# Performance work log

Measured on AMD Instinct MI355X. Metric: run time of the kernel, lower is better.

## Reference

```python
import jax, jax.numpy as jnp
import numpy as np

ALPHA = 0.2  # LeakyReLU slope
S1, S2 = 5, 10  # neighbor sample sizes, hard-coded in the torch forward

N, F, D, C, B = 100000, 512, 256, 40, 16384


def setup_inputs() -> dict:
    key = jax.random.key(0)
    ks = jax.random.split(key, 7)
    x = jax.random.normal(ks[0], (N, F), dtype=jnp.float32)
    # xavier-like scaling for the weights
    W1 = jax.random.normal(ks[1], (D, F), dtype=jnp.float32) * (2.0 / (D + F)) ** 0.5
    W2 = jax.random.normal(ks[2], (D, D), dtype=jnp.float32) * (2.0 / (D + D)) ** 0.5
    Wc = jax.random.normal(ks[3], (C, D), dtype=jnp.float32) * (2.0 / (C + D)) ** 0.5
    nodes = jax.random.randint(ks[4], (B,), 0, N, dtype=jnp.int32)
    neigh1 = jax.random.randint(ks[5], (N, S1), 0, N, dtype=jnp.int32)
    neigh2 = jax.random.randint(ks[6], (B, S2), 0, N, dtype=jnp.int32)
    return {"x": x, "W1": W1, "W2": W2, "Wc": Wc,
            "nodes": nodes, "neigh1": neigh1, "neigh2": neigh2}


def leaky_relu(v):
    return jnp.where(v >= 0, v, ALPHA * v)


def reference(x, W1, W2, Wc, nodes, neigh1, neigh2):
    # Layer 1 (MeanAggregator, gcn=True): mean over sampled neighbors + self,
    # then linear transform + LeakyReLU. Computed for all N nodes.
    agg1 = (x[neigh1].sum(axis=1) + x) / (S1 + 1)          # [N, F]
    h1 = leaky_relu(agg1 @ W1.T)                            # [N, D]
    # Layer 2: mean over sampled neighbors + self, on batch nodes.
    agg2 = (h1[neigh2].sum(axis=1) + h1[nodes]) / (S2 + 1)  # [B, D]
    h2 = leaky_relu(agg2 @ W2.T)                            # [B, D]
    # scores = self.weight.mm(x_2.t()).t()
    scores = h2 @ Wc.T                                      # [B, C]
    return scores
```

## Files before the change

### kernel.cpp

```cpp
#include <hip/hip_runtime.h>
#include <hip/hip_bf16.h>


#define NN 100000
#define FF 512
#define DD 256
#define BB 16384
#define CC 40

typedef __attribute__((ext_vector_type(8))) short bf16x8;
typedef __attribute__((ext_vector_type(4))) float f32x4;
typedef unsigned short u16;
typedef unsigned int u32;
typedef __attribute__((ext_vector_type(4))) u32 u32x4;

__device__ __forceinline__ float bf_lo(u32 u) { u32 v = u << 16; float f; __builtin_memcpy(&f, &v, 4); return f; }
__device__ __forceinline__ float bf_hi(u32 u) { u32 v = u & 0xffff0000u; float f; __builtin_memcpy(&f, &v, 4); return f; }
__device__ __forceinline__ float2 bf2f(u32 u) { return make_float2(bf_lo(u), bf_hi(u)); }
__device__ __forceinline__ float asf(u32 u) { float f; __builtin_memcpy(&f, &u, 4); return f; }
__device__ __forceinline__ u32 packbf2(float a, float b) {
  __hip_bfloat162 h = __float22bfloat162_rn(make_float2(a, b));
  u32 u; __builtin_memcpy(&u, &h, 4); return u;
}
__device__ __forceinline__ u16 fbits(float v) {
  __hip_bfloat16 h = __float2bfloat16(v);
  u16 u; __builtin_memcpy(&u, &h, 2); return u;
}
__device__ __forceinline__ float lrelu(float v) { return v >= 0.f ? v : 0.2f * v; }
__device__ __forceinline__ int swz(int r, int c) { return r * 128 + ((c ^ (r & 7)) << 4); }
__device__ __forceinline__ void gld_lds16(const u16* g, void* l) {
  __builtin_amdgcn_global_load_lds((const __attribute__((address_space(1))) unsigned int*)g,
                                   (__attribute__((address_space(3))) unsigned int*)l, 16, 0, 0);
}
__device__ __forceinline__ u32x4 ld4(const float* p) { return *(const u32x4*)p; }

__global__ __launch_bounds__(256) void k0_cvt(
    const float* __restrict__ W1, const float* __restrict__ W2, const float* __restrict__ Wc,
    u16* __restrict__ w1b, u16* __restrict__ w2b, u16* __restrict__ wcb,
    u32* __restrict__ flagw)
{
  const int i = blockIdx.x * 256 + threadIdx.x;
  if (i < 25024) flagw[i] = 0;
  const float* src; u16* dst; int r, cc, rowE;
  if (i < 16384)      { src = W1; dst = w1b; r = i >> 6; cc = i & 63; rowE = 512; }
  else if (i < 24576) { int j = i - 16384; src = W2; dst = w2b; r = j >> 5; cc = j & 31; rowE = 256; }
  else if (i < 25856) { int j = i - 24576; src = Wc; dst = wcb; r = j >> 5; cc = j & 31; rowE = 256; }
  else return;
  const int g = cc >> 3, cp = cc & 7;
  const float* s = src + (u32)r * rowE + g * 64 + (u32)(cp ^ (r & 7)) * 8;
  const float4 v0 = *(const float4*)s;
  const float4 v1 = *(const float4*)(s + 4);
  uint4 o;
  o.x = packbf2(v0.x, v0.y); o.y = packbf2(v0.z, v0.w);
  o.z = packbf2(v1.x, v1.y); o.w = packbf2(v1.z, v1.w);
  *(uint4*)(dst + (u32)r * rowE + g * 64 + cp * 8) = o;
}

__global__ __launch_bounds__(256) void k0b_flags(
    const int* __restrict__ nodes, const int* __restrict__ neigh2,
    unsigned char* __restrict__ flags)
{
  const int i = blockIdx.x * 256 + threadIdx.x;
  int idx;
  if (i < BB) idx = nodes[i];
  else if (i < BB + BB * 10) idx = neigh2[i - BB];
  else return;
  flags[idx] = 1;
}

__global__ __launch_bounds__(512, 4) void k1_gemm(
    const float* __restrict__ x, const u16* __restrict__ w1b, u16* __restrict__ z)
{
  __shared__ __align__(16) unsigned char lds[65536];

  const int t = threadIdx.x;
  const int rowBase = blockIdx.x * 128;
  const int lane = t & 63, w = t >> 6;
  const int lr = lane & 15, kg = lane >> 4;

  int rw = rowBase + w * 16 + lr; if (rw > NN - 1) rw = NN - 1;
  const float* xr = x + (u32)rw * FF + (u32)kg * 8;

  const u32 bofs = (u32)(w * 8 + (lane >> 3)) * FF + (u32)(lane & 7) * 8;

  int bvb[2];
#pragma unroll
  for (int kk = 0; kk < 2; ++kk)
    bvb[kk] = lr * 128 + (((kk * 4 + kg) ^ (lr & 7)) << 4);

  f32x4 acc[16];
#pragma unroll
  for (int n = 0; n < 16; ++n) acc[n] = (f32x4)0.0f;

  u32x4 pa[2][2];
#pragma unroll
  for (int kk = 0; kk < 2; ++kk) {
    pa[kk][0] = ld4(xr + kk * 32);
    pa[kk][1] = ld4(xr + kk * 32 + 4);
  }
#pragma unroll
  for (int i = 0; i < 4; ++i)
    gld_lds16(w1b + bofs + (u32)i * 64 * FF, lds + w * 1024 + i * 8192);
#pragma unroll
  for (int i = 0; i < 4; ++i)
    gld_lds16(w1b + bofs + (u32)i * 64 * FF + 64, lds + 32768 + w * 1024 + i * 8192);

#pragma unroll
  for (int ks = 0; ks < 8; ++ks) {
    bf16x8 av[2];
#pragma unroll
    for (int kk = 0; kk < 2; ++kk) {
      u32x4 p;
      p[0] = packbf2(asf(pa[kk][0][0]), asf(pa[kk][0][1]));
      p[1] = packbf2(asf(pa[kk][0][2]), asf(pa[kk][0][3]));
      p[2] = packbf2(asf(pa[kk][1][0]), asf(pa[kk][1][1]));
      p[3] = packbf2(asf(pa[kk][1][2]), asf(pa[kk][1][3]));
      av[kk] = *(bf16x8*)&p;
    }
    if (ks < 7) {
#pragma unroll
      for (int kk = 0; kk < 2; ++kk) {
        pa[kk][0] = ld4(xr + (u32)(ks + 1) * 64 + kk * 32);
        pa[kk][1] = ld4(xr + (u32)(ks + 1) * 64 + kk * 32 + 4);
      }
      asm volatile("s_waitcnt vmcnt(8)" ::: "memory");
    } else {
      asm volatile("s_waitcnt vmcnt(0)" ::: "memory");
    }
    __builtin_amdgcn_sched_barrier(0);
    __builtin_amdgcn_s_barrier();
    __builtin_amdgcn_sched_barrier(0);

    const int bo = (ks & 1) * 32768;
#pragma unroll
    for (int kk = 0; kk < 2; ++kk)
#pragma unroll
      for (int n = 0; n < 16; ++n) {
        const bf16x8 bv = *(const bf16x8*)(lds + bo + bvb[kk] + n * 2048);
        acc[n] = __builtin_amdgcn_mfma_f32_16x16x32_bf16(bv, av[kk], acc[n], 0, 0, 0);
      }
    __builtin_amdgcn_sched_barrier(0);
    __builtin_amdgcn_s_barrier();
    __builtin_amdgcn_sched_barrier(0);
    if (ks <= 5) {
      unsigned char* bl = lds + bo + w * 1024;
#pragma unroll
      for (int i = 0; i < 4; ++i)
        gld_lds16(w1b + bofs + (u32)i * 64 * FF + (u32)(ks + 2) * 64, bl + i * 8192);
    }
  }

  __syncthreads();
  {
    const int zr = w * 16 + lr;
#pragma unroll
    for (int n = 0; n < 16; ++n) {
      const int zc = n * 16 + kg * 4;
      uint2 o;
      o.x = packbf2(acc[n][0], acc[n][1]);
      o.y = packbf2(acc[n][2], acc[n][3]);
      const int ch = zc >> 3;
      const int pch = (ch & 24) | ((ch ^ (zr & 7)) & 7);
      *(uint2*)(lds + zr * 512 + pch * 16 + (zc & 7) * 2) = o;
    }
  }
  __syncthreads();
#pragma unroll
  for (int i = 0; i < 8; ++i) {
    const int id = t + i * 512;
    const int rr = id >> 5, cc = id & 31;
    const int pch = (cc & 24) | ((cc ^ (rr & 7)) & 7);
    const uint4 v = *(const uint4*)(lds + rr * 512 + pch * 16);
    *(uint4*)(z + (u32)(rowBase + rr) * DD + cc * 8) = v;
  }
}

__global__ __launch_bounds__(256) void k2_agg1(
    const u16* __restrict__ z, const int* __restrict__ neigh1, u16* __restrict__ h1,
    const unsigned char* __restrict__ flags)
{
  const int t = threadIdx.x;
  const int row = blockIdx.x * 8 + (t >> 5);
  if (!flags[row]) return;
  const int ch = t & 31;
  const u32 o0 = (u32)row * DD + ch * 8;
  uint4 a = *(const uint4*)(z + o0);
  float2 s0 = bf2f(a.x), s1 = bf2f(a.y), s2 = bf2f(a.z), s3 = bf2f(a.w);
#pragma unroll
  for (int j = 0; j < 5; ++j) {
    const int idx = neigh1[row * 5 + j];
    const uint4 v = *(const uint4*)(z + (u32)idx * DD + ch * 8);
    s0.x += bf_lo(v.x); s0.y += bf_hi(v.x);
    s1.x += bf_lo(v.y); s1.y += bf_hi(v.y);
    s2.x += bf_lo(v.z); s2.y += bf_hi(v.z);
    s3.x += bf_lo(v.w); s3.y += bf_hi(v.w);
  }
  const float sc = 1.0f / 6.0f;
  uint4 o;
  o.x = packbf2(lrelu(s0.x * sc), lrelu(s0.y * sc));
  o.y = packbf2(lrelu(s1.x * sc), lrelu(s1.y * sc));
  o.z = packbf2(lrelu(s2.x * sc), lrelu(s2.y * sc));
  o.w = packbf2(lrelu(s3.x * sc), lrelu(s3.y * sc));
  *(uint4*)(h1 + o0) = o;
}

__global__ __launch_bounds__(512, 2) void k3_fused(
    const u16* __restrict__ h1, const u16* __restrict__ w2b, const u16* __restrict__ wcb,
    const int* __restrict__ nodes, const int* __restrict__ neigh2, float* __restrict__ out)
{
  __shared__ __align__(16) unsigned char lds[65536];

  const int t = threadIdx.x;
  const int rowBase = blockIdx.x * 64;
  const int lane = t & 63, w = t >> 6;
  const int wm = w >> 2, wn = w & 3;
  const int lr = lane & 15, kg = lane >> 4;

#pragma unroll
  for (int i = 0; i < 3; ++i) {
    const int id = t + i * 512;
    uint4 v = make_uint4(0u, 0u, 0u, 0u);
    if (id < 1280) v = *(const uint4*)(wcb + (u32)id * 8);
    *(uint4*)(lds + 40960 + id * 16) = v;
  }

  const int r = t >> 3, c = t & 7;
  const int b = rowBase + r;
  u32 offA[11];
  offA[0] = (u32)nodes[b] * DD + (u32)c * 8;
#pragma unroll
  for (int j = 0; j < 10; ++j)
    offA[1 + j] = (u32)neigh2[b * 10 + j] * DD + (u32)c * 8;
  const int aW = swz(r, c);

  const u32 bofs = (u32)(w * 8 + (lane >> 3)) * DD + (u32)(lane & 7) * 8;
  unsigned char* bl0 = lds + 8192 + w * 1024;

  int aA[2][2], bA[2][4];
#pragma unroll
  for (int kk = 0; kk < 2; ++kk) {
    const int cb = kk * 4 + kg;
#pragma unroll
    for (int m = 0; m < 2; ++m) aA[kk][m] = swz(wm * 32 + m * 16 + lr, cb);
#pragma unroll
    for (int n = 0; n < 4; ++n) bA[kk][n] = 8192 + swz(wn * 64 + n * 16 + lr, cb);
  }

  f32x4 acc[2][4];
#pragma unroll
  for (int m = 0; m < 2; ++m)
#pragma unroll
    for (int n = 0; n < 4; ++n) acc[m][n] = (f32x4)0.0f;

  uint4 ag[11];
#pragma unroll
  for (int j = 0; j < 11; ++j) ag[j] = *(const uint4*)(h1 + offA[j]);

  for (int ks = 0; ks < 4; ++ks) {
    if (ks) __builtin_amdgcn_s_barrier();
    {
      float2 s0 = make_float2(0.f, 0.f), s1 = make_float2(0.f, 0.f);
      float2 s2 = make_float2(0.f, 0.f), s3 = make_float2(0.f, 0.f);
#pragma unroll
      for (int j = 0; j < 11; ++j) {
        s0.x += bf_lo(ag[j].x); s0.y += bf_hi(ag[j].x);
        s1.x += bf_lo(ag[j].y); s1.y += bf_hi(ag[j].y);
        s2.x += bf_lo(ag[j].z); s2.y += bf_hi(ag[j].z);
        s3.x += bf_lo(ag[j].w); s3.y += bf_hi(ag[j].w);
      }
      const float sc = 1.0f / 11.0f;
      uint4 o;
      o.x = packbf2(s0.x * sc, s0.y * sc);
      o.y = packbf2(s1.x * sc, s1.y * sc);
      o.z = packbf2(s2.x * sc, s2.y * sc);
      o.w = packbf2(s3.x * sc, s3.y * sc);
      *(uint4*)(lds + aW) = o;
    }
#pragma unroll
    for (int i = 0; i < 4; ++i)
      gld_lds16(w2b + bofs + (u32)i * 64 * DD + (u32)ks * 64, bl0 + i * 8192);
    __syncthreads();
    if (ks < 3) {
#pragma unroll
      for (int j = 0; j < 11; ++j)
        ag[j] = *(const uint4*)(h1 + offA[j] + (u32)(ks + 1) * 64);
    }
    __builtin_amdgcn_sched_barrier(0);
#pragma unroll
    for (int kk = 0; kk < 2; ++kk) {
      bf16x8 av[2], bv[4];
#pragma unroll
      for (int m = 0; m < 2; ++m) av[m] = *(const bf16x8*)(lds + aA[kk][m]);
#pragma unroll
      for (int n = 0; n < 4; ++n) bv[n] = *(const bf16x8*)(lds + bA[kk][n]);
#pragma unroll
      for (int m = 0; m < 2; ++m)
#pragma unroll
        for (int n = 0; n < 4; ++n)
          acc[m][n] = __builtin_amdgcn_mfma_f32_16x16x32_bf16(av[m], bv[n], acc[m][n], 0, 0, 0);
    }
  }

  __syncthreads();
#pragma unroll
  for (int m = 0; m < 2; ++m) {
#pragma unroll
    for (int j = 0; j < 4; ++j) {
      const int row = wm * 32 + m * 16 + kg * 4 + j;
#pragma unroll
      for (int n = 0; n < 4; ++n) {
        const int col = wn * 64 + n * 16 + lr;
        const int ch = col >> 3;
        const int pch = (ch & 24) | ((ch ^ row) & 7);
        *(u16*)(lds + row * 512 + pch * 16 + (col & 7) * 2) = fbits(lrelu(acc[m][n][j]));
      }
    }
  }
  __syncthreads();

  if (w < 4) {
    f32x4 acc2[3];
#pragma unroll
    for (int n = 0; n < 3; ++n) acc2[n] = (f32x4)0.0f;
    const int arow = w * 16 + lr;
#pragma unroll
    for (int ks2 = 0; ks2 < 8; ++ks2) {
      const int chb = ks2 * 4 + kg;
      const int pchA = (chb & 24) | ((chb ^ arow) & 7);
      const bf16x8 a = *(const bf16x8*)(lds + arow * 512 + pchA * 16);
#pragma unroll
      for (int n = 0; n < 3; ++n) {
        const int brow = n * 16 + lr;
        const int pchB = (chb & 24) | ((chb ^ brow) & 7);
        const bf16x8 bb = *(const bf16x8*)(lds + 40960 + brow * 512 + pchB * 16);
        acc2[n] = __builtin_amdgcn_mfma_f32_16x16x32_bf16(a, bb, acc2[n], 0, 0, 0);
      }
    }
#pragma unroll
    for (int n = 0; n < 3; ++n) {
      const int col = n * 16 + lr;
      if (col < CC) {
#pragma unroll
        for (int j = 0; j < 4; ++j) {
          const int rr = rowBase + w * 16 + kg * 4 + j;
          out[(u32)rr * CC + col] = acc2[n][j];
        }
      }
    }
  }
}

extern "C" void kernel_launch(void* const* d_in, const int* in_sizes, int n_in,
                              void* d_out, int out_size, void* d_ws, size_t ws_size,
                              hipStream_t stream) {
  const float* x    = (const float*)d_in[0];
  const float* W1   = (const float*)d_in[1];
  const float* W2   = (const float*)d_in[2];
  const float* Wc   = (const float*)d_in[3];
  const int* nodes  = (const int*)d_in[4];
  const int* neigh1 = (const int*)d_in[5];
  const int* neigh2 = (const int*)d_in[6];

  u16* z   = (u16*)d_ws;
  u16* h1  = z + (size_t)100096 * 256;
  u16* w1b = h1 + (size_t)100096 * 256;
  u16* w2b = w1b + (size_t)256 * 512;
  u16* wcb = w2b + (size_t)256 * 256;
  u32* flagw = (u32*)(wcb + (size_t)40 * 256);
  unsigned char* flags = (unsigned char*)flagw;

  k0_cvt<<<dim3(101), dim3(256), 0, stream>>>(W1, W2, Wc, w1b, w2b, wcb, flagw);
  k0b_flags<<<dim3(704), dim3(256), 0, stream>>>(nodes, neigh2, flags);
  k1_gemm<<<dim3(782), dim3(512), 0, stream>>>(x, w1b, z);
  k2_agg1<<<dim3(12500), dim3(256), 0, stream>>>(z, neigh1, h1, flags);
  k3_fused<<<dim3(256), dim3(512), 0, stream>>>(h1, w2b, wcb, nodes, neigh2, (float*)d_out);
}
```

Before: 128.8 us.

## Halve k1 GEMM tile to 64 rows and K-step to 32 with new W1 swizzle

```diff
diff --git a/kernel.cpp b/kernel.cpp
--- a/kernel.cpp
+++ b/kernel.cpp
@@ -41,19 +41,30 @@
 {
   const int i = blockIdx.x * 256 + threadIdx.x;
   if (i < 25024) flagw[i] = 0;
-  const float* src; u16* dst; int r, cc, rowE;
-  if (i < 16384)      { src = W1; dst = w1b; r = i >> 6; cc = i & 63; rowE = 512; }
-  else if (i < 24576) { int j = i - 16384; src = W2; dst = w2b; r = j >> 5; cc = j & 31; rowE = 256; }
-  else if (i < 25856) { int j = i - 24576; src = Wc; dst = wcb; r = j >> 5; cc = j & 31; rowE = 256; }
+  if (i < 16384) {
+    const int r = i >> 6, cc = i & 63;
+    const int lc = (cc & ~3) | ((cc ^ r) & 3);
+    const float* s = W1 + (u32)r * 512 + (u32)lc * 8;
+    const float4 v0 = *(const float4*)s;
+    const float4 v1 = *(const float4*)(s + 4);
+    uint4 o;
+    o.x = packbf2(v0.x, v0.y); o.y = packbf2(v0.z, v0.w);
+    o.z = packbf2(v1.x, v1.y); o.w = packbf2(v1.z, v1.w);
+    *(uint4*)(w1b + (u32)r * 512 + (u32)cc * 8) = o;
+    return;
+  }
+  const float* src; u16* dst; int r, cc;
+  if (i < 24576)      { int j = i - 16384; src = W2; dst = w2b; r = j >> 5; cc = j & 31; }
+  else if (i < 25856) { int j = i - 24576; src = Wc; dst = wcb; r = j >> 5; cc = j & 31; }
   else return;
   const int g = cc >> 3, cp = cc & 7;
-  const float* s = src + (u32)r * rowE + g * 64 + (u32)(cp ^ (r & 7)) * 8;
+  const float* s = src + (u32)r * 256 + g * 64 + (u32)(cp ^ (r & 7)) * 8;
   const float4 v0 = *(const float4*)s;
   const float4 v1 = *(const float4*)(s + 4);
   uint4 o;
   o.x = packbf2(v0.x, v0.y); o.y = packbf2(v0.z, v0.w);
   o.z = packbf2(v1.x, v1.y); o.w = packbf2(v1.z, v1.w);
-  *(uint4*)(dst + (u32)r * rowE + g * 64 + cp * 8) = o;
+  *(uint4*)(dst + (u32)r * 256 + g * 64 + cp * 8) = o;
 }
 
 __global__ __launch_bounds__(256) void k0b_flags(
@@ -68,62 +79,52 @@
   flags[idx] = 1;
 }
 
-__global__ __launch_bounds__(512, 4) void k1_gemm(
+__global__ __launch_bounds__(256, 4) void k1_gemm(
     const float* __restrict__ x, const u16* __restrict__ w1b, u16* __restrict__ z)
 {
-  __shared__ __align__(16) unsigned char lds[65536];
+  __shared__ __align__(16) unsigned char lds[32768];
 
   const int t = threadIdx.x;
-  const int rowBase = blockIdx.x * 128;
+  const int rowBase = blockIdx.x * 64;
   const int lane = t & 63, w = t >> 6;
   const int lr = lane & 15, kg = lane >> 4;
 
   int rw = rowBase + w * 16 + lr; if (rw > NN - 1) rw = NN - 1;
   const float* xr = x + (u32)rw * FF + (u32)kg * 8;
 
-  const u32 bofs = (u32)(w * 8 + (lane >> 3)) * FF + (u32)(lane & 7) * 8;
-
-  int bvb[2];
-#pragma unroll
-  for (int kk = 0; kk < 2; ++kk)
-    bvb[kk] = lr * 128 + (((kk * 4 + kg) ^ (lr & 7)) << 4);
+  const u32 bofs = (u32)(w * 16 + (lane >> 2)) * FF + (u32)(lane & 3) * 8;
+
+  const int bvb = lr * 64 + ((kg ^ (lr & 3)) << 4);
 
   f32x4 acc[16];
 #pragma unroll
   for (int n = 0; n < 16; ++n) acc[n] = (f32x4)0.0f;
 
-  u32x4 pa[2][2];
-#pragma unroll
-  for (int kk = 0; kk < 2; ++kk) {
-    pa[kk][0] = ld4(xr + kk * 32);
-    pa[kk][1] = ld4(xr + kk * 32 + 4);
-  }
+  u32x4 pa[2];
+  pa[0] = ld4(xr);
+  pa[1] = ld4(xr + 4);
 #pragma unroll
   for (int i = 0; i < 4; ++i)
-    gld_lds16(w1b + bofs + (u32)i * 64 * FF, lds + w * 1024 + i * 8192);
+    gld_lds16(w1b + bofs + (u32)i * 64 * FF, lds + w * 1024 + i * 4096);
 #pragma unroll
   for (int i = 0; i < 4; ++i)
-    gld_lds16(w1b + bofs + (u32)i * 64 * FF + 64, lds + 32768 + w * 1024 + i * 8192);
-
-#pragma unroll
-  for (int ks = 0; ks < 8; ++ks) {
-    bf16x8 av[2];
-#pragma unroll
-    for (int kk = 0; kk < 2; ++kk) {
+    gld_lds16(w1b + bofs + (u32)i * 64 * FF + 32, lds + 16384 + w * 1024 + i * 4096);
+
+#pragma unroll 2
+  for (int ks = 0; ks < 16; ++ks) {
+    bf16x8 av;
+    {
       u32x4 p;
-      p[0] = packbf2(asf(pa[kk][0][0]), asf(pa[kk][0][1]));
-      p[1] = packbf2(asf(pa[kk][0][2]), asf(pa[kk][0][3]));
-      p[2] = packbf2(asf(pa[kk][1][0]), asf(pa[kk][1][1]));
-      p[3] = packbf2(asf(pa[kk][1][2]), asf(pa[kk][1][3]));
-      av[kk] = *(bf16x8*)&p;
-    }
-    if (ks < 7) {
-#pragma unroll
-      for (int kk = 0; kk < 2; ++kk) {
-        pa[kk][0] = ld4(xr + (u32)(ks + 1) * 64 + kk * 32);
-        pa[kk][1] = ld4(xr + (u32)(ks + 1) * 64 + kk * 32 + 4);
-      }
-      asm volatile("s_waitcnt vmcnt(8)" ::: "memory");
+      p[0] = packbf2(asf(pa[0][0]), asf(pa[0][1]));
+      p[1] = packbf2(asf(pa[0][2]), asf(pa[0][3]));
+      p[2] = packbf2(asf(pa[1][0]), asf(pa[1][1]));
+      p[3] = packbf2(asf(pa[1][2]), asf(pa[1][3]));
+      av = *(bf16x8*)&p;
+    }
+    if (ks < 15) {
+      pa[0] = ld4(xr + (u32)(ks + 1) * 32);
+      pa[1] = ld4(xr + (u32)(ks + 1) * 32 + 4);
+      asm volatile("s_waitcnt vmcnt(6)" ::: "memory");
     } else {
       asm volatile("s_waitcnt vmcnt(0)" ::: "memory");
     }
@@ -131,22 +132,20 @@
     __builtin_amdgcn_s_barrier();
     __builtin_amdgcn_sched_barrier(0);
 
-    const int bo = (ks & 1) * 32768;
-#pragma unroll
-    for (int kk = 0; kk < 2; ++kk)
-#pragma unroll
-      for (int n = 0; n < 16; ++n) {
-        const bf16x8 bv = *(const bf16x8*)(lds + bo + bvb[kk] + n * 2048);
-        acc[n] = __builtin_amdgcn_mfma_f32_16x16x32_bf16(bv, av[kk], acc[n], 0, 0, 0);
-      }
+    const int bo = (ks & 1) * 16384;
+#pragma unroll
+    for (int n = 0; n < 16; ++n) {
+      const bf16x8 bv = *(const bf16x8*)(lds + bo + bvb + n * 1024);
+      acc[n] = __builtin_amdgcn_mfma_f32_16x16x32_bf16(bv, av, acc[n], 0, 0, 0);
+    }
     __builtin_amdgcn_sched_barrier(0);
     __builtin_amdgcn_s_barrier();
     __builtin_amdgcn_sched_barrier(0);
-    if (ks <= 5) {
+    if (ks <= 13) {
       unsigned char* bl = lds + bo + w * 1024;
 #pragma unroll
       for (int i = 0; i < 4; ++i)
-        gld_lds16(w1b + bofs + (u32)i * 64 * FF + (u32)(ks + 2) * 64, bl + i * 8192);
+        gld_lds16(w1b + bofs + (u32)i * 64 * FF + (u32)(ks + 2) * 32, bl + i * 4096);
     }
   }
 
@@ -167,7 +166,7 @@
   __syncthreads();
 #pragma unroll
   for (int i = 0; i < 8; ++i) {
-    const int id = t + i * 512;
+    const int id = t + i * 256;
     const int rr = id >> 5, cc = id & 31;
     const int pch = (cc & 24) | ((cc ^ (rr & 7)) & 7);
     const uint4 v = *(const uint4*)(lds + rr * 512 + pch * 16);
@@ -371,7 +370,7 @@
 
   k0_cvt<<<dim3(101), dim3(256), 0, stream>>>(W1, W2, Wc, w1b, w2b, wcb, flagw);
   k0b_flags<<<dim3(704), dim3(256), 0, stream>>>(nodes, neigh2, flags);
-  k1_gemm<<<dim3(782), dim3(512), 0, stream>>>(x, w1b, z);
+  k1_gemm<<<dim3(1563), dim3(256), 0, stream>>>(x, w1b, z);
   k2_agg1<<<dim3(12500), dim3(256), 0, stream>>>(z, neigh1, h1, flags);
   k3_fused<<<dim3(256), dim3(512), 0, stream>>>(h1, w2b, wcb, nodes, neigh2, (float*)d_out);
 }
```

New measurement: 155.4 us. +20.7%, slower.
